# Optimization experiments

Measured on AMD Instinct MI355X. Metric: run time of the kernel, lower is better.

Reference implementation:

```python
import jax, jax.numpy as jnp
import numpy as np

B, L, S, D_MODEL, H = 4, 2048, 2048, 512, 8
E = D_MODEL // H  # head dim = 64


def setup_inputs() -> dict:
    key = jax.random.key(0)
    ks = jax.random.split(key, 11)
    s = 1.0 / np.sqrt(D_MODEL)
    return {
        "queries": jax.random.normal(ks[0], (B, L, D_MODEL), jnp.float32),
        "keys": jax.random.normal(ks[1], (B, S, D_MODEL), jnp.float32),
        "values": jax.random.normal(ks[2], (B, S, D_MODEL), jnp.float32),
        "Wq": jax.random.normal(ks[3], (D_MODEL, D_MODEL), jnp.float32) * s,
        "bq": jnp.zeros((D_MODEL,), jnp.float32),
        "Wk": jax.random.normal(ks[4], (D_MODEL, D_MODEL), jnp.float32) * s,
        "bk": jnp.zeros((D_MODEL,), jnp.float32),
        "Wv": jax.random.normal(ks[5], (D_MODEL, D_MODEL), jnp.float32) * s,
        "bv": jnp.zeros((D_MODEL,), jnp.float32),
        "Wo": jax.random.normal(ks[6], (D_MODEL, D_MODEL), jnp.float32) * s,
        "bo": jnp.zeros((D_MODEL,), jnp.float32),
    }


def reference(queries, keys, values, Wq, bq, Wk, bk, Wv, bv, Wo, bo):
    # QKV projections, then split heads: [B, T, H, E]
    q = (queries @ Wq + bq).reshape(B, L, H, E)
    k = (keys @ Wk + bk).reshape(B, S, H, E)
    v = (values @ Wv + bv).reshape(B, S, H, E)
    scale = 1.0 / np.sqrt(E)
    # Naive full attention: materialized [B, H, L, S] scores (as in original)
    scores = jnp.einsum('blhe,bshe->bhls', q, k)
    A = jax.nn.softmax(scale * scores, axis=-1)  # dropout = identity at eval
    out = jnp.einsum('bhls,bshd->blhd', A, v).reshape(B, L, H * E)
    return out @ Wo + bo
```

## Files before the change

### kernel.cpp

```cpp
#include <hip/hip_runtime.h>
#include <hip/hip_bf16.h>


typedef __attribute__((ext_vector_type(8))) short bf8_t;
typedef __attribute__((ext_vector_type(4))) float f4_t;
typedef __attribute__((ext_vector_type(16))) float f16_t;
typedef __attribute__((ext_vector_type(4))) unsigned int u32x4;

#define D_MODEL 512
#define HEADS 8
#define EDIM 64
#define LSEQ 2048
#define NBATCH 4
#define MTOT (NBATCH * LSEQ)

static __device__ __forceinline__ unsigned short f2bf(float f) {
  union { float f; unsigned int u; } x;
  x.f = f;
  unsigned int u = x.u;
  u += 0x7FFFu + ((u >> 16) & 1u);
  return (unsigned short)(u >> 16);
}

static __device__ __forceinline__ unsigned int pack2bf(float a, float b) {
  union { __hip_bfloat162 h; unsigned int u; } c;
  c.h.x = __float2bfloat16(a);
  c.h.y = __float2bfloat16(b);
  return c.u;
}

#define GLOAD_LDS(gptr, lptr)                                                        \
  __builtin_amdgcn_global_load_lds((const __attribute__((address_space(1))) void*)(gptr), \
                                   (__attribute__((address_space(3))) void*)(lptr), 16, 0, 0)

__global__ void wt_cvt_all(const float* __restrict__ Wq, const float* __restrict__ Wk,
                           const float* __restrict__ Wv, const float* __restrict__ Wo,
                           unsigned short* __restrict__ Wqt, unsigned short* __restrict__ Wkt,
                           unsigned short* __restrict__ Wvt, unsigned short* __restrict__ Wot) {
  __shared__ float tile[64][65];
  const int which = blockIdx.z;
  const float* W = (which == 0) ? Wq : (which == 1) ? Wk : (which == 2) ? Wv : Wo;
  unsigned short* Wt = (which == 0) ? Wqt : (which == 1) ? Wkt : (which == 2) ? Wvt : Wot;
  const int k0 = blockIdx.x * 64, n0 = blockIdx.y * 64;
  const int tx = threadIdx.x & 63;
  const int ty = threadIdx.x >> 6;
#pragma unroll
  for (int i = 0; i < 64; i += 4)
    tile[i + ty][tx] = W[(size_t)(k0 + i + ty) * D_MODEL + n0 + tx];
  __syncthreads();
#pragma unroll
  for (int i = 0; i < 64; i += 4)
    Wt[(size_t)(n0 + i + ty) * D_MODEL + k0 + tx] = f2bf(tile[tx][i + ty]);
}

__device__ __forceinline__ void stage_a_f32(const float* __restrict__ A, float* lA,
                                            int m0, int k0) {
  const int t = threadIdx.x;
#pragma unroll
  for (int ii = 0; ii < 2; ++ii) {
    int c = t + ii * 256;
    int row = c >> 3, col = c & 7;
    int colp = col ^ (row & 7);
    GLOAD_LDS((const char*)(A + (size_t)(m0 + row) * D_MODEL + k0 + colp * 4),
              (char*)lA + c * 16);
  }
}
__device__ __forceinline__ void stage_a_bf16(const unsigned short* __restrict__ A,
                                             unsigned short* lA, int m0, int k0) {
  const int t = threadIdx.x;
  int rowA = t >> 2, cbA = (t & 3) * 16;
  GLOAD_LDS((const char*)(A + (size_t)(m0 + rowA) * D_MODEL + k0) + cbA, (char*)lA + t * 16);
}
__device__ __forceinline__ void stage_b(const unsigned short* __restrict__ Bt,
                                        unsigned short* lB, int n0, int k0) {
  const int t = threadIdx.x;
#pragma unroll
  for (int ii = 0; ii < 2; ++ii) {
    int c = t + ii * 256;
    int rowB = c >> 2, cbB = (c & 3) * 16;
    GLOAD_LDS((const char*)(Bt + (size_t)(n0 + rowB) * D_MODEL + k0) + cbB, (char*)lB + c * 16);
  }
}

template <bool AF32>
__device__ __forceinline__ void gemm_core(const void* __restrict__ Av,
                                          const unsigned short* __restrict__ Bt,
                                          void* __restrict__ lAv,
                                          unsigned short* __restrict__ lBv,
                                          f4_t (&acc)[2][4], int m0, int n0) {
  const int t = threadIdx.x;
  const int lane = t & 63;
  const int w = t >> 6;
  const int wr = w >> 1, wc = w & 1;
  const int r = lane & 15, g = lane >> 4;
  const int ASZ = 64 * 32;

  if constexpr (AF32) stage_a_f32((const float*)Av, (float*)lAv, m0, 0);
  else                stage_a_bf16((const unsigned short*)Av, (unsigned short*)lAv, m0, 0);
  stage_b(Bt, lBv, n0, 0);
  __syncthreads();

  int cur = 0;
  const int NK = D_MODEL / 32;
  for (int ks = 0; ks < NK; ++ks) {
    if (ks + 1 < NK) {
      const int kn = (ks + 1) * 32;
      if constexpr (AF32)
        stage_a_f32((const float*)Av, (float*)lAv + (cur ^ 1) * ASZ, m0, kn);
      else
        stage_a_bf16((const unsigned short*)Av, (unsigned short*)lAv + (cur ^ 1) * ASZ, m0, kn);
      stage_b(Bt, lBv + (cur ^ 1) * 128 * 32, n0, kn);
    }

    bf8_t af[2], bfv[4];
    if constexpr (AF32) {
      const float* lA = (const float*)lAv + cur * ASZ;
#pragma unroll
      for (int mi = 0; mi < 2; ++mi) {
        const int row = wr * 32 + mi * 16 + r;
        const f4_t lo = *(const f4_t*)(lA + row * 32 + (((2 * g + 0) ^ (row & 7)) << 2));
        const f4_t hi4 = *(const f4_t*)(lA + row * 32 + (((2 * g + 1) ^ (row & 7)) << 2));
        union { unsigned int u[4]; bf8_t b; } pb;
        pb.u[0] = pack2bf(lo[0], lo[1]);
        pb.u[1] = pack2bf(lo[2], lo[3]);
        pb.u[2] = pack2bf(hi4[0], hi4[1]);
        pb.u[3] = pack2bf(hi4[2], hi4[3]);
        af[mi] = pb.b;
      }
    } else {
      const unsigned short* lA = (const unsigned short*)lAv + cur * ASZ;
#pragma unroll
      for (int mi = 0; mi < 2; ++mi)
        af[mi] = *(const bf8_t*)(lA + (wr * 32 + mi * 16 + r) * 32 + g * 8);
    }
    const unsigned short* lB = lBv + cur * 128 * 32;
#pragma unroll
    for (int ni = 0; ni < 4; ++ni)
      bfv[ni] = *(const bf8_t*)(lB + (wc * 64 + ni * 16 + r) * 32 + g * 8);
#pragma unroll
    for (int mi = 0; mi < 2; ++mi)
#pragma unroll
      for (int ni = 0; ni < 4; ++ni)
        acc[mi][ni] = __builtin_amdgcn_mfma_f32_16x16x32_bf16(af[mi], bfv[ni], acc[mi][ni], 0, 0, 0);
    __syncthreads();
    cur ^= 1;
  }
}

#define QSCALE 0.18033688011112042f
__global__ __launch_bounds__(256, 4) void qkv_gemm(
    const float* __restrict__ Xq, const float* __restrict__ Xk, const float* __restrict__ Xv,
    const unsigned short* __restrict__ Wqt, const unsigned short* __restrict__ Wkt,
    const unsigned short* __restrict__ Wvt,
    const float* __restrict__ bq, const float* __restrict__ bk, const float* __restrict__ bv,
    unsigned short* __restrict__ Qh, unsigned short* __restrict__ Kh,
    unsigned short* __restrict__ Vt) {
  __shared__ alignas(16) float lA[2][64 * 32];
  __shared__ alignas(16) unsigned short lB[2][128 * 32];
  const int z = blockIdx.z;
  const float* A           = (z == 0) ? Xq : (z == 1) ? Xk : Xv;
  const unsigned short* Bt = (z == 0) ? Wqt : (z == 1) ? Wkt : Wvt;
  const float* bias        = (z == 0) ? bq : (z == 1) ? bk : bv;
  const int n0 = blockIdx.x * 128, m0 = blockIdx.y * 64;

  f4_t acc[2][4] = {};
  gemm_core<true>(A, Bt, &lA[0][0], &lB[0][0], acc, m0, n0);

  const int lane = threadIdx.x & 63;
  const int w = threadIdx.x >> 6;
  const int wr = w >> 1, wc = w & 1;
  const int r = lane & 15, g = lane >> 4;
#pragma unroll
  for (int mi = 0; mi < 2; ++mi)
#pragma unroll
    for (int ni = 0; ni < 4; ++ni) {
      const int coln = n0 + wc * 64 + ni * 16 + r;
      const float bv_ = bias[coln];
      const int h = coln >> 6, e = coln & 63;
#pragma unroll
      for (int j = 0; j < 4; ++j) {
        const int rowm = m0 + wr * 32 + mi * 16 + g * 4 + j;
        const int b = rowm >> 11, li = rowm & 2047;
        float v = acc[mi][ni][j] + bv_;
        if (z == 0) {
          v *= QSCALE;
          Qh[(((size_t)(b * HEADS + h) * LSEQ + li) << 6) + e] = f2bf(v);
        } else if (z == 1) {
          Kh[(((size_t)(b * HEADS + h) * LSEQ + li) << 6) + e] = f2bf(v);
        } else {
          Vt[(((size_t)(b * HEADS + h) * EDIM + e) << 11) + li] = f2bf(v);
        }
      }
    }
}

__global__ __launch_bounds__(256, 4) void o_gemm(const unsigned short* __restrict__ A,
                                                 const unsigned short* __restrict__ Bt,
                                                 const float* __restrict__ bias,
                                                 float* __restrict__ Cout) {
  __shared__ alignas(16) unsigned short lA[2][64 * 32];
  __shared__ alignas(16) unsigned short lB[2][128 * 32];
  const int n0 = blockIdx.x * 128, m0 = blockIdx.y * 64;
  f4_t acc[2][4] = {};
  gemm_core<false>(A, Bt, &lA[0][0], &lB[0][0], acc, m0, n0);

  const int lane = threadIdx.x & 63;
  const int w = threadIdx.x >> 6;
  const int wr = w >> 1, wc = w & 1;
  const int r = lane & 15, g = lane >> 4;
#pragma unroll
  for (int mi = 0; mi < 2; ++mi)
#pragma unroll
    for (int ni = 0; ni < 4; ++ni) {
      const int coln = n0 + wc * 64 + ni * 16 + r;
      const float bv_ = bias[coln];
#pragma unroll
      for (int j = 0; j < 4; ++j) {
        const int rowm = m0 + wr * 32 + mi * 16 + g * 4 + j;
        Cout[(size_t)rowm * D_MODEL + coln] = acc[mi][ni][j] + bv_;
      }
    }
}

#define XSTR 68

__device__ __forceinline__ void stage_tile(const unsigned short* __restrict__ Kbase,
                                           const unsigned short* __restrict__ Vbase,
                                           unsigned short* ldsK, unsigned short* ldsV,
                                           int s0, int tg) {
#pragma unroll
  for (int ii = 0; ii < 2; ++ii) {
    int c = tg + ii * 256;
    int row = c >> 3, col = c & 7;
    int colp = col ^ (row & 7);
    GLOAD_LDS((const char*)(Kbase + (size_t)(s0 + row) * EDIM + colp * 8),
              (char*)ldsK + c * 16);
    GLOAD_LDS((const char*)(Vbase + (size_t)row * LSEQ + s0 + colp * 8),
              (char*)ldsV + c * 16);
  }
}

__global__ __launch_bounds__(512, 4) void flash_attn(const unsigned short* __restrict__ Qh,
                                                     const unsigned short* __restrict__ Kh,
                                                     const unsigned short* __restrict__ Vt,
                                                     unsigned short* __restrict__ Ao) {
  __shared__ alignas(16) unsigned short stg[2][2][2][64 * 64];

  const int t = threadIdx.x;
  const int lane = t & 63;
  const int w = t >> 6;
  const int wg = w >> 2;
  const int wq = w & 3;
  const int tg = t & 255;
  const int qn = lane & 31;
  const int hi = lane >> 5;
  const int bh = blockIdx.y;
  const int q0 = blockIdx.x * 128 + wq * 32;
  const int sbase = wg * (LSEQ / 2);

  bf8_t qf[4];
#pragma unroll
  for (int kst = 0; kst < 4; ++kst)
    qf[kst] = *(const bf8_t*)(Qh + ((size_t)bh * LSEQ + q0 + qn) * EDIM + kst * 16 + hi * 8);

  float l_lane = 0.f;
  f16_t oacc[2];
#pragma unroll
  for (int eh = 0; eh < 2; ++eh)
#pragma unroll
    for (int r = 0; r < 16; ++r) oacc[eh][r] = 0.f;

  const unsigned short* Kbase = Kh + (size_t)bh * LSEQ * EDIM;
  const unsigned short* Vbase = Vt + (size_t)bh * EDIM * LSEQ;

  stage_tile(Kbase, Vbase, stg[wg][0][0], stg[wg][0][1], sbase, tg);
  __syncthreads();

  int cur = 0;
  const int NT = LSEQ / 2 / 64;
  for (int kt = 0; kt < NT; ++kt) {
    if (kt + 1 < NT)
      stage_tile(Kbase, Vbase, stg[wg][cur ^ 1][0], stg[wg][cur ^ 1][1],
                 sbase + (kt + 1) * 64, tg);

    const unsigned short* lsK = stg[wg][cur][0];
    const unsigned short* lsV = stg[wg][cur][1];

    bf8_t kf[2][4];
#pragma unroll
    for (int sh = 0; sh < 2; ++sh)
#pragma unroll
      for (int kst = 0; kst < 4; ++kst) {
        const int row = 32 * sh + qn;
        const int ch = (2 * kst + hi) ^ (row & 7);
        kf[sh][kst] = *(const bf8_t*)(&lsK[row * 64 + ch * 8]);
      }
    f16_t sacc[2];
#pragma unroll
    for (int sh = 0; sh < 2; ++sh)
#pragma unroll
      for (int r = 0; r < 16; ++r) sacc[sh][r] = 0.f;
#pragma unroll
    for (int sh = 0; sh < 2; ++sh)
#pragma unroll
      for (int kst = 0; kst < 4; ++kst)
        sacc[sh] = __builtin_amdgcn_mfma_f32_32x32x16_bf16(kf[sh][kst], qf[kst], sacc[sh], 0, 0, 0);

    unsigned int pk[16];
#pragma unroll
    for (int sh = 0; sh < 2; ++sh)
#pragma unroll
      for (int i = 0; i < 8; ++i) {
        const float a = __builtin_amdgcn_exp2f(sacc[sh][2 * i]);
        const float b = __builtin_amdgcn_exp2f(sacc[sh][2 * i + 1]);
        l_lane += a + b;
        pk[sh * 8 + i] = pack2bf(a, b);
      }

    unsigned int sw[16];
#pragma unroll
    for (int i = 0; i < 16; ++i) sw[i] = __shfl_xor(pk[i], 32);

    bf8_t pvb[4];
#pragma unroll
    for (int t2 = 0; t2 < 4; ++t2) {
      union { u32x4 u; bf8_t b; } pb;
      pb.u[0] = hi ? sw[4 * t2 + 2] : pk[4 * t2 + 0];
      pb.u[1] = hi ? sw[4 * t2 + 3] : pk[4 * t2 + 1];
      pb.u[2] = hi ? pk[4 * t2 + 2] : sw[4 * t2 + 0];
      pb.u[3] = hi ? pk[4 * t2 + 3] : sw[4 * t2 + 1];
      pvb[t2] = pb.b;
    }

#pragma unroll
    for (int eh = 0; eh < 2; ++eh)
#pragma unroll
      for (int t2 = 0; t2 < 4; ++t2) {
        const int row = 32 * eh + qn;
        const int ch = (2 * t2 + hi) ^ (row & 7);
        const bf8_t vf = *(const bf8_t*)(&lsV[row * 64 + ch * 8]);
        oacc[eh] = __builtin_amdgcn_mfma_f32_32x32x16_bf16(vf, pvb[t2], oacc[eh], 0, 0, 0);
      }

    __syncthreads();
    cur ^= 1;
  }

  const float l_own = l_lane + __shfl_xor(l_lane, 32);
  float* xO = (float*)&stg[0][0][0][0];
  float* xL = xO + 128 * XSTR;

  if (wg == 1) {
#pragma unroll
    for (int eh = 0; eh < 2; ++eh)
#pragma unroll
      for (int k = 0; k < 4; ++k) {
        float4 v4;
        v4.x = oacc[eh][4 * k + 0]; v4.y = oacc[eh][4 * k + 1];
        v4.z = oacc[eh][4 * k + 2]; v4.w = oacc[eh][4 * k + 3];
        *(float4*)(xO + (wq * 32 + qn) * XSTR + 32 * eh + 8 * k + 4 * hi) = v4;
      }
    if (hi == 0) xL[wq * 32 + qn] = l_own;
  }
  __syncthreads();

  if (wg == 0) {
    const float inv = 1.f / (l_own + xL[wq * 32 + qn]);
    const int b = bh >> 3, h = bh & 7;
#pragma unroll
    for (int eh = 0; eh < 2; ++eh)
#pragma unroll
      for (int k = 0; k < 4; ++k) {
        const float4 v4 = *(const float4*)(xO + (wq * 32 + qn) * XSTR + 32 * eh + 8 * k + 4 * hi);
        ushort4 ov;
        ov.x = f2bf((oacc[eh][4 * k + 0] + v4.x) * inv);
        ov.y = f2bf((oacc[eh][4 * k + 1] + v4.y) * inv);
        ov.z = f2bf((oacc[eh][4 * k + 2] + v4.z) * inv);
        ov.w = f2bf((oacc[eh][4 * k + 3] + v4.w) * inv);
        const int e = 32 * eh + 8 * k + 4 * hi;
        *(ushort4*)(Ao + ((size_t)(b * LSEQ + q0 + qn)) * D_MODEL + h * EDIM + e) = ov;
      }
  }
}

extern "C" void kernel_launch(void* const* d_in, const int* in_sizes, int n_in,
                              void* d_out, int out_size, void* d_ws, size_t ws_size,
                              hipStream_t stream) {
  const float* queries = (const float*)d_in[0];
  const float* keys    = (const float*)d_in[1];
  const float* values  = (const float*)d_in[2];
  const float* Wq = (const float*)d_in[3];
  const float* bq = (const float*)d_in[4];
  const float* Wk = (const float*)d_in[5];
  const float* bk = (const float*)d_in[6];
  const float* Wv = (const float*)d_in[7];
  const float* bv = (const float*)d_in[8];
  const float* Wo = (const float*)d_in[9];
  const float* bo = (const float*)d_in[10];

  char* ws = (char*)d_ws;
  const size_t XSZ = (size_t)MTOT * D_MODEL * 2;
  unsigned short* Qh  = (unsigned short*)(ws + 3 * XSZ);
  unsigned short* Kh  = (unsigned short*)(ws + 4 * XSZ);
  unsigned short* Vt  = (unsigned short*)(ws + 5 * XSZ);
  unsigned short* Ao  = (unsigned short*)(ws + 6 * XSZ);
  unsigned short* Wqt = (unsigned short*)(ws + 7 * XSZ);
  unsigned short* Wkt = Wqt + 512 * 512;
  unsigned short* Wvt = Wkt + 512 * 512;
  unsigned short* Wot = Wvt + 512 * 512;

  wt_cvt_all<<<dim3(8, 8, 4), 256, 0, stream>>>(Wq, Wk, Wv, Wo, Wqt, Wkt, Wvt, Wot);

  qkv_gemm<<<dim3(D_MODEL / 128, MTOT / 64, 3), 256, 0, stream>>>(
      queries, keys, values, Wqt, Wkt, Wvt, bq, bk, bv, Qh, Kh, Vt);

  flash_attn<<<dim3(LSEQ / 128, NBATCH * HEADS), 512, 0, stream>>>(Qh, Kh, Vt, Ao);

  o_gemm<<<dim3(D_MODEL / 128, MTOT / 64), 256, 0, stream>>>(Ao, Wot, bo, (float*)d_out);
}
```

Before: 114.2 us.

## Triple-buffer GEMM LDS staging with vmcnt waits and remap block order

The projection GEMM core moves from double to triple buffering. It prefetches two K-steps ahead and uses explicit s_waitcnt vmcnt plus raw s_barrier instead of __syncthreads, so global-to-LDS loads overlap more with MFMA work. Both GEMM kernels now launch a 1D grid with a swizzled block index, so neighbouring blocks share A rows across the four N tiles, aiming for better L2 reuse. The costs are 1.5x LDS per block, which may lower occupancy, and hand-tuned vmcnt counts that must match the number of loads each stage issues.

```diff
diff --git a/kernel.cpp b/kernel.cpp
--- a/kernel.cpp
+++ b/kernel.cpp
@@ -93,28 +93,40 @@
   const int w = t >> 6;
   const int wr = w >> 1, wc = w & 1;
   const int r = lane & 15, g = lane >> 4;
-  const int ASZ = 64 * 32;
-
-  if constexpr (AF32) stage_a_f32((const float*)Av, (float*)lAv, m0, 0);
-  else                stage_a_bf16((const unsigned short*)Av, (unsigned short*)lAv, m0, 0);
-  stage_b(Bt, lBv, n0, 0);
-  __syncthreads();
-
-  int cur = 0;
+  const int ASZ = 64 * 32, BSZ = 128 * 32;
   const int NK = D_MODEL / 32;
+
+  if constexpr (AF32) {
+    stage_a_f32((const float*)Av, (float*)lAv + 0 * ASZ, m0, 0);
+    stage_b(Bt, lBv + 0 * BSZ, n0, 0);
+    stage_a_f32((const float*)Av, (float*)lAv + 1 * ASZ, m0, 32);
+    stage_b(Bt, lBv + 1 * BSZ, n0, 32);
+    asm volatile("s_waitcnt vmcnt(4)" ::: "memory");
+  } else {
+    stage_a_bf16((const unsigned short*)Av, (unsigned short*)lAv + 0 * ASZ, m0, 0);
+    stage_b(Bt, lBv + 0 * BSZ, n0, 0);
+    stage_a_bf16((const unsigned short*)Av, (unsigned short*)lAv + 1 * ASZ, m0, 32);
+    stage_b(Bt, lBv + 1 * BSZ, n0, 32);
+    asm volatile("s_waitcnt vmcnt(3)" ::: "memory");
+  }
+  __builtin_amdgcn_s_barrier();
+  __builtin_amdgcn_sched_barrier(0);
+
   for (int ks = 0; ks < NK; ++ks) {
-    if (ks + 1 < NK) {
-      const int kn = (ks + 1) * 32;
+    const int cb = ks % 3;
+    const bool more = (ks + 2 < NK);
+    if (more) {
+      const int nb = (ks + 2) % 3, kn = (ks + 2) * 32;
       if constexpr (AF32)
-        stage_a_f32((const float*)Av, (float*)lAv + (cur ^ 1) * ASZ, m0, kn);
+        stage_a_f32((const float*)Av, (float*)lAv + nb * ASZ, m0, kn);
       else
-        stage_a_bf16((const unsigned short*)Av, (unsigned short*)lAv + (cur ^ 1) * ASZ, m0, kn);
-      stage_b(Bt, lBv + (cur ^ 1) * 128 * 32, n0, kn);
+        stage_a_bf16((const unsigned short*)Av, (unsigned short*)lAv + nb * ASZ, m0, kn);
+      stage_b(Bt, lBv + nb * BSZ, n0, kn);
     }
 
     bf8_t af[2], bfv[4];
     if constexpr (AF32) {
-      const float* lA = (const float*)lAv + cur * ASZ;
+      const float* lA = (const float*)lAv + cb * ASZ;
 #pragma unroll
       for (int mi = 0; mi < 2; ++mi) {
         const int row = wr * 32 + mi * 16 + r;
@@ -128,12 +140,12 @@
         af[mi] = pb.b;
       }
     } else {
-      const unsigned short* lA = (const unsigned short*)lAv + cur * ASZ;
+      const unsigned short* lA = (const unsigned short*)lAv + cb * ASZ;
 #pragma unroll
       for (int mi = 0; mi < 2; ++mi)
         af[mi] = *(const bf8_t*)(lA + (wr * 32 + mi * 16 + r) * 32 + g * 8);
     }
-    const unsigned short* lB = lBv + cur * 128 * 32;
+    const unsigned short* lB = lBv + cb * BSZ;
 #pragma unroll
     for (int ni = 0; ni < 4; ++ni)
       bfv[ni] = *(const bf8_t*)(lB + (wc * 64 + ni * 16 + r) * 32 + g * 8);
@@ -142,8 +154,15 @@
 #pragma unroll
       for (int ni = 0; ni < 4; ++ni)
         acc[mi][ni] = __builtin_amdgcn_mfma_f32_16x16x32_bf16(af[mi], bfv[ni], acc[mi][ni], 0, 0, 0);
-    __syncthreads();
-    cur ^= 1;
+
+    if (more) {
+      if constexpr (AF32) asm volatile("s_waitcnt vmcnt(4)" ::: "memory");
+      else                asm volatile("s_waitcnt vmcnt(3)" ::: "memory");
+    } else {
+      asm volatile("s_waitcnt vmcnt(0)" ::: "memory");
+    }
+    __builtin_amdgcn_s_barrier();
+    __builtin_amdgcn_sched_barrier(0);
   }
 }
 
@@ -155,13 +174,19 @@
     const float* __restrict__ bq, const float* __restrict__ bk, const float* __restrict__ bv,
     unsigned short* __restrict__ Qh, unsigned short* __restrict__ Kh,
     unsigned short* __restrict__ Vt) {
-  __shared__ alignas(16) float lA[2][64 * 32];
-  __shared__ alignas(16) unsigned short lB[2][128 * 32];
-  const int z = blockIdx.z;
+  __shared__ alignas(16) float lA[3][64 * 32];
+  __shared__ alignas(16) unsigned short lB[3][128 * 32];
+  const int p = blockIdx.x;
+  const int res = p & 7, q = p >> 3;
+  const int xx = q & 3;
+  const int grp = res + ((q >> 2) << 3);
+  const int z = grp >> 7;
+  const int y = grp & 127;
+  const int n0 = xx * 128, m0 = y * 64;
+
   const float* A           = (z == 0) ? Xq : (z == 1) ? Xk : Xv;
   const unsigned short* Bt = (z == 0) ? Wqt : (z == 1) ? Wkt : Wvt;
   const float* bias        = (z == 0) ? bq : (z == 1) ? bk : bv;
-  const int n0 = blockIdx.x * 128, m0 = blockIdx.y * 64;
 
   f4_t acc[2][4] = {};
   gemm_core<true>(A, Bt, &lA[0][0], &lB[0][0], acc, m0, n0);
@@ -198,9 +223,14 @@
                                                  const unsigned short* __restrict__ Bt,
                                                  const float* __restrict__ bias,
                                                  float* __restrict__ Cout) {
-  __shared__ alignas(16) unsigned short lA[2][64 * 32];
-  __shared__ alignas(16) unsigned short lB[2][128 * 32];
-  const int n0 = blockIdx.x * 128, m0 = blockIdx.y * 64;
+  __shared__ alignas(16) unsigned short lA[3][64 * 32];
+  __shared__ alignas(16) unsigned short lB[3][128 * 32];
+  const int p = blockIdx.x;
+  const int res = p & 7, q = p >> 3;
+  const int xx = q & 3;
+  const int grp = res + ((q >> 2) << 3);
+  const int n0 = xx * 128, m0 = grp * 64;
+
   f4_t acc[2][4] = {};
   gemm_core<false>(A, Bt, &lA[0][0], &lB[0][0], acc, m0, n0);
 
@@ -411,10 +441,10 @@
 
   wt_cvt_all<<<dim3(8, 8, 4), 256, 0, stream>>>(Wq, Wk, Wv, Wo, Wqt, Wkt, Wvt, Wot);
 
-  qkv_gemm<<<dim3(D_MODEL / 128, MTOT / 64, 3), 256, 0, stream>>>(
+  qkv_gemm<<<1536, 256, 0, stream>>>(
       queries, keys, values, Wqt, Wkt, Wvt, bq, bk, bv, Qh, Kh, Vt);
 
   flash_attn<<<dim3(LSEQ / 128, NBATCH * HEADS), 512, 0, stream>>>(Qh, Kh, Vt, Ao);
 
-  o_gemm<<<dim3(D_MODEL / 128, MTOT / 64), 256, 0, stream>>>(Ao, Wot, bo, (float*)d_out);
-}
+  o_gemm<<<512, 256, 0, stream>>>(Ao, Wot, bo, (float*)d_out);
+}
```

Result: faster. 109.6 us (-4.0%).
